# Optimization experiments

Hardware: AMD Instinct MI355X
Metric: run time of the kernel (lower is better)

Reference implementation:

```python
import jax, jax.numpy as jnp
import numpy as np

N = 100000   # nodes
E = 1600000  # edges
R = 500      # relation types
D = 128      # in_ent_feats == out_ent_feats
H = 8        # heads
Dh = 16      # head dim
DFF = 4 * D  # feed-forward hidden
HOPS = 5
ALPHA = 0.15
SLOPE = 0.2
EPS = 1e-5


def setup_inputs() -> dict:
    key = jax.random.key(0)
    ks = jax.random.split(key, 12)
    s = 0.05  # small-init scale
    return {
        "ent_feat": jax.random.normal(ks[0], (N, D), jnp.float32),
        "rel_feat": jax.random.normal(ks[1], (R, D), jnp.float32),
        "src": jax.random.randint(ks[2], (E,), 0, N),
        "dst": jax.random.randint(ks[3], (E,), 0, N),
        "e_type": jax.random.randint(ks[4], (E,), 0, R),
        "ln1_g": jnp.ones((D,), jnp.float32),
        "ln1_b": jnp.zeros((D,), jnp.float32),
        "W_ent": jax.random.normal(ks[5], (D, H * Dh), jnp.float32) * s,
        "W_rel": jax.random.normal(ks[6], (D, H * Dh), jnp.float32) * s,
        "attn_h": jax.random.normal(ks[7], (1, H, Dh), jnp.float32) * s,
        "attn_t": jax.random.normal(ks[8], (1, H, Dh), jnp.float32) * s,
        "attn_r": jax.random.normal(ks[9], (1, H, Dh), jnp.float32) * s,
        "ln2_g": jnp.ones((H * Dh,), jnp.float32),
        "ln2_b": jnp.zeros((H * Dh,), jnp.float32),
        "W1": jax.random.normal(ks[10], (H * Dh, DFF), jnp.float32) * s,
        "b1": jnp.zeros((DFF,), jnp.float32),
        "W2": jax.random.normal(ks[11], (DFF, H * Dh), jnp.float32) * s,
        "b2": jnp.zeros((H * Dh,), jnp.float32),
    }


def _ln(x, g, b):
    mu = x.mean(-1, keepdims=True)
    var = x.var(-1, keepdims=True)
    return (x - mu) * jax.lax.rsqrt(var + EPS) * g + b


def reference(ent_feat, rel_feat, src, dst, e_type,
              ln1_g, ln1_b, W_ent, W_rel, attn_h, attn_t, attn_r,
              ln2_g, ln2_b, W1, b1, W2, b2):
    # graph layer norm (dropout is identity at eval)
    h = _ln(ent_feat, ln1_g, ln1_b)                       # [N, D]
    feat = (h @ W_ent).reshape(N, H, Dh)                  # [N, H, Dh]
    frel = (rel_feat @ W_rel).reshape(R, H, Dh)           # [R, H, Dh]
    eh = (feat * attn_h).sum(-1)                          # [N, H]
    et = (feat * attn_t).sum(-1)                          # [N, H]
    er = (frel * attn_r).sum(-1)[e_type]                  # [E, H]
    # edge scores: u_add_v + relation term, leaky relu
    e = eh[src] + et[dst] + er                            # [E, H]
    e = jnp.where(e > 0, e, SLOPE * e)
    # edge softmax over incoming edges of each dst node
    m = jax.ops.segment_max(e, dst, num_segments=N)       # [N, H]
    ex = jnp.exp(e - m[dst])
    ssum = jax.ops.segment_sum(ex, dst, num_segments=N)
    a = ex / ssum[dst]                                    # [E, H]
    # PPR diffusion
    feat0 = feat
    f = feat0
    for _ in range(HOPS):
        msg = f[src] * a[:, :, None]                      # [E, H, Dh]
        agg = jax.ops.segment_sum(msg, dst, num_segments=N)
        f = (1.0 - ALPHA) * agg + ALPHA * feat0
    # residual (Identity since in == out)
    rst = f + h.reshape(N, H, Dh)
    rst = rst.reshape(N, H * Dh)
    # feed-forward sublayer with residual
    y = _ln(rst, ln2_g, ln2_b)
    ff = jax.nn.relu(y @ W1 + b1) @ W2 + b2
    return ff + rst
```

## Files before the change

kernel.cpp:

```cpp
#include <hip/hip_runtime.h>
#include <hip/hip_bf16.h>
#include <math.h>

#define N_NODES 100000
#define N_EDGES 1600000
#define N_REL   500
#define DIM     128
#define NHEAD   8
#define DFF     512
#define ALPHA   0.15f
#define SLOPE   0.2f
#define LN_EPS  1e-5f

#define SCHUNK   1024
#define NSCANBLK ((N_NODES + SCHUNK - 1) / SCHUNK)

typedef unsigned short u16;
typedef unsigned int   u32;

typedef __attribute__((ext_vector_type(8))) short  bf16x8;
typedef __attribute__((ext_vector_type(4))) float  f32x4;

__device__ __forceinline__ float bf2f(u16 u) {
    return __uint_as_float(((u32)u) << 16);
}
__device__ __forceinline__ u16 f2bf(float f) {
    __hip_bfloat16 b = __float2bfloat16(f);
    return *reinterpret_cast<u16*>(&b);
}
__device__ __forceinline__ u32 pack2(float a, float b) {
    return (u32)f2bf(a) | ((u32)f2bf(b) << 16);
}

__global__ void zero_k(int* __restrict__ p, int n) {
    int i = blockIdx.x * blockDim.x + threadIdx.x;
    if (i < n) p[i] = 0;
}

__global__ void swz1_k(const float* __restrict__ W1, u16* __restrict__ W1s) {
    const int i = blockIdx.x * 256 + threadIdx.x;
    const int k = i >> 9, n = i & 511;
    W1s[n * DIM + k] = f2bf(W1[i]);
}
__global__ void swz2_k(const float* __restrict__ W2, u16* __restrict__ W2s) {
    const int i = blockIdx.x * 256 + threadIdx.x;
    const int k = i >> 7, n = i & 127;
    W2s[n * DFF + k] = f2bf(W2[i]);
}
__global__ void swze_k(const float* __restrict__ W, u16* __restrict__ Ws) {
    const int i = blockIdx.x * 256 + threadIdx.x;
    const int k = i >> 7, n = i & 127;
    Ws[n * DIM + k] = f2bf(W[i]);
}

__global__ __launch_bounds__(128) void ln1_k(const float* __restrict__ x,
        const float* __restrict__ g, const float* __restrict__ b,
        float* __restrict__ h) {
    const int n = blockIdx.x, t = threadIdx.x;
    const float v = x[n * DIM + t];
    float s = v, q = v * v;
#pragma unroll
    for (int off = 32; off > 0; off >>= 1) {
        s += __shfl_xor(s, off, 64);
        q += __shfl_xor(q, off, 64);
    }
    __shared__ float ss[2], qq[2];
    if ((t & 63) == 0) { ss[t >> 6] = s; qq[t >> 6] = q; }
    __syncthreads();
    s = ss[0] + ss[1]; q = qq[0] + qq[1];
    const float mu  = s * (1.0f / 128.0f);
    const float var = q * (1.0f / 128.0f) - mu * mu;
    const float rs  = rsqrtf(fmaxf(var, 0.f) + LN_EPS);
    h[n * DIM + t] = (v - mu) * rs * g[t] + b[t];
}

#define HP 136
__global__ __launch_bounds__(256) void proj_k(const float* __restrict__ h,
        const u16* __restrict__ Wes,
        u16* __restrict__ feat0) {
    __shared__ u16 hsb[32 * HP];
    const int t   = threadIdx.x;
    const int n0b = blockIdx.x * 32;

    {
        const int sr = t >> 3;
        const int sc = (t & 7) * 16;
        const float* hrow = &h[(size_t)(n0b + sr) * DIM + sc];
        u16* drow = &hsb[sr * HP + sc];
#pragma unroll
        for (int i = 0; i < 4; ++i) {
            const float4 hv = ((const float4*)hrow)[i];
            ushort4 o;
            o.x = f2bf(hv.x); o.y = f2bf(hv.y); o.z = f2bf(hv.z); o.w = f2bf(hv.w);
            ((ushort4*)drow)[i] = o;
        }
    }
    __syncthreads();

    const int wv   = t >> 6;
    const int lane = t & 63;
    const int lm   = lane & 15;
    const int q4   = lane >> 4;
    const int mrow = (wv & 1) * 16;
    const int chalf = (wv >> 1) * 64;

    bf16x8 afr[4];
#pragma unroll
    for (int kt = 0; kt < 4; ++kt)
        afr[kt] = *(const bf16x8*)&hsb[(mrow + lm) * HP + kt * 32 + q4 * 8];

#pragma unroll
    for (int nt = 0; nt < 4; ++nt) {
        const int c0 = chalf + nt * 16;
        f32x4 acc = {0.f, 0.f, 0.f, 0.f};
#pragma unroll
        for (int kt = 0; kt < 4; ++kt) {
            const bf16x8 bfr = *(const bf16x8*)&Wes[(c0 + lm) * DIM + kt * 32 + q4 * 8];
            acc = __builtin_amdgcn_mfma_f32_16x16x32_bf16(afr[kt], bfr, acc, 0, 0, 0);
        }
#pragma unroll
        for (int r = 0; r < 4; ++r)
            feat0[(size_t)(n0b + mrow + q4 * 4 + r) * DIM + c0 + lm] = f2bf(acc[r]);
    }
}

__global__ __launch_bounds__(256) void eh_k(const u16* __restrict__ feat0,
        const float* __restrict__ attn_h, const float* __restrict__ attn_t,
        float* __restrict__ eh, float* __restrict__ et) {
    __shared__ float ahs[DIM], ats[DIM];
    const int t = threadIdx.x;
    if (t < DIM) { ahs[t] = attn_h[t]; ats[t] = attn_t[t]; }
    __syncthreads();
    const int idx  = blockIdx.x * 256 + t;
    const int n    = idx >> 3;
    const int head = idx & 7;
    const u16* fp = &feat0[(size_t)n * DIM + head * 16];
    float sh = 0.f, st = 0.f;
#pragma unroll
    for (int i = 0; i < 4; ++i) {
        const ushort4 f4 = ((const ushort4*)fp)[i];
        const int c = head * 16 + i * 4;
        sh += bf2f(f4.x) * ahs[c+0] + bf2f(f4.y) * ahs[c+1]
            + bf2f(f4.z) * ahs[c+2] + bf2f(f4.w) * ahs[c+3];
        st += bf2f(f4.x) * ats[c+0] + bf2f(f4.y) * ats[c+1]
            + bf2f(f4.z) * ats[c+2] + bf2f(f4.w) * ats[c+3];
    }
    eh[idx] = sh;
    et[idx] = st;
}

__global__ __launch_bounds__(128) void rel_k(const float* __restrict__ rel_feat,
        const float* __restrict__ W,
        const float* __restrict__ attn_r, float* __restrict__ er) {
    __shared__ float rf[DIM];
    __shared__ float pr[DIM];
    const int r = blockIdx.x, t = threadIdx.x;
    rf[t] = rel_feat[r * DIM + t];
    __syncthreads();
    float acc = 0.f;
    for (int d = 0; d < DIM; ++d) acc += rf[d] * W[d * DIM + t];
    pr[t] = acc * attn_r[t];
    __syncthreads();
    if (t < NHEAD) {
        float s = 0.f;
        for (int i = 0; i < 16; ++i) s += pr[t * 16 + i];
        er[r * NHEAD + t] = s;
    }
}

__global__ void count_k(const int* __restrict__ dst, int* __restrict__ counts) {
    int e = blockIdx.x * blockDim.x + threadIdx.x;
    if (e < N_EDGES) atomicAdd(&counts[dst[e]], 1);
}

__global__ __launch_bounds__(256) void scan1_k(const int* __restrict__ counts,
        int* __restrict__ offsets, int* __restrict__ blk_sums, int n) {
    __shared__ int wsum[4];
    const int t = threadIdx.x, lane = t & 63, wid = t >> 6;
    const int base = blockIdx.x * SCHUNK + t * 4;
    int v0 = 0, v1 = 0, v2 = 0, v3 = 0;
    if (base + 3 < n) {
        const int4 c4 = *(const int4*)&counts[base];
        v0 = c4.x; v1 = c4.y; v2 = c4.z; v3 = c4.w;
    } else {
        if (base + 0 < n) v0 = counts[base + 0];
        if (base + 1 < n) v1 = counts[base + 1];
        if (base + 2 < n) v2 = counts[base + 2];
        if (base + 3 < n) v3 = counts[base + 3];
    }
    const int s4 = v0 + v1 + v2 + v3;
    int incl = s4;
#pragma unroll
    for (int off = 1; off < 64; off <<= 1) {
        const int tt = __shfl_up(incl, off, 64);
        if (lane >= off) incl += tt;
    }
    if (lane == 63) wsum[wid] = incl;
    __syncthreads();
    int wbase = 0;
#pragma unroll
    for (int w = 0; w < 4; ++w) if (w < wid) wbase += wsum[w];
    const int excl = wbase + incl - s4;
    if (base + 0 < n) offsets[base + 0] = excl;
    if (base + 1 < n) offsets[base + 1] = excl + v0;
    if (base + 2 < n) offsets[base + 2] = excl + v0 + v1;
    if (base + 3 < n) offsets[base + 3] = excl + v0 + v1 + v2;
    if (t == 255) blk_sums[blockIdx.x] = wbase + incl;
}

__global__ __launch_bounds__(128) void scan2_k(const int* __restrict__ blk_sums,
        int* __restrict__ blk_off, int* __restrict__ offsets, int nblk, int n) {
    const int t = threadIdx.x;
    const int v = (t < nblk) ? blk_sums[t] : 0;
    int incl = v;
#pragma unroll
    for (int off = 1; off < 64; off <<= 1) {
        const int tt = __shfl_up(incl, off, 64);
        if ((t & 63) >= off) incl += tt;
    }
    __shared__ int w0sum;
    if (t == 63) w0sum = incl;
    __syncthreads();
    int x = incl - v;
    if (t >= 64) x += w0sum;
    if (t < nblk) blk_off[t] = x;
    if (t == nblk - 1) offsets[n] = x + v;
}

__global__ __launch_bounds__(256) void scan3_k(int* __restrict__ offsets,
        int* __restrict__ cursor, const int* __restrict__ blk_off, int n) {
    const int add  = blk_off[blockIdx.x];
    const int base = blockIdx.x * SCHUNK + threadIdx.x * 4;
#pragma unroll
    for (int j = 0; j < 4; ++j) {
        const int i = base + j;
        if (i < n) {
            const int o = offsets[i] + add;
            offsets[i] = o;
            cursor[i]  = o;
        }
    }
}

__global__ void scatter_k(const int* __restrict__ src, const int* __restrict__ dst,
        const int* __restrict__ etype,
        int* __restrict__ cursor, u32* __restrict__ csr_se) {
    const int e = blockIdx.x * blockDim.x + threadIdx.x;
    if (e >= N_EDGES) return;
    const int s = src[e], d = dst[e], r = etype[e];
    const int pos = atomicAdd(&cursor[d], 1);
    if (pos < 0 || pos >= N_EDGES) return;
    csr_se[pos] = (u32)s | ((u32)r << 17);
}

__global__ __launch_bounds__(256) void softmax_k(const int* __restrict__ offsets,
        const u32* __restrict__ csr_se,
        const float* __restrict__ eh, const float* __restrict__ et,
        const float* __restrict__ er,
        u16* __restrict__ csr_ab, float* __restrict__ inv_buf) {
    const int n = blockIdx.x * 4 + (threadIdx.x >> 6);
    const int beg = offsets[n], end = offsets[n + 1];
    const int lane = threadIdx.x & 63;
    const int k  = lane & 7;
    const int eo = lane >> 3;
    const float etk = et[n * NHEAD + k];
    float m = -1e30f;
    for (int e = beg + eo; e < end; e += 8) {
        const u32 se = csr_se[e];
        const int s = se & 0x1FFFF;
        const int r = se >> 17;
        float sc = eh[s * NHEAD + k] + etk + er[r * NHEAD + k];
        sc = sc > 0.f ? sc : SLOPE * sc;
        m = fmaxf(m, sc);
    }
    m = fmaxf(m, __shfl_xor(m, 8, 64));
    m = fmaxf(m, __shfl_xor(m, 16, 64));
    m = fmaxf(m, __shfl_xor(m, 32, 64));
    float ssum = 0.f;
    for (int e = beg + eo; e < end; e += 8) {
        const u32 se = csr_se[e];
        const int s = se & 0x1FFFF;
        const int r = se >> 17;
        float sc = eh[s * NHEAD + k] + etk + er[r * NHEAD + k];
        sc = sc > 0.f ? sc : SLOPE * sc;
        const float ex = expf(sc - m);
        csr_ab[(size_t)e * NHEAD + k] = f2bf(ex);
        ssum += ex;
    }
    ssum += __shfl_xor(ssum, 8, 64);
    ssum += __shfl_xor(ssum, 16, 64);
    ssum += __shfl_xor(ssum, 32, 64);
    const float inv = 1.f / fmaxf(ssum, 1e-20f);
    if (lane < 8) inv_buf[n * NHEAD + lane] = inv;
}

__global__ __launch_bounds__(256) void hop_k(const u16* __restrict__ f_in,
        u16* __restrict__ f_out, const u16* __restrict__ feat0,
        const int* __restrict__ offsets, const u32* __restrict__ csr_se,
        const u16* __restrict__ csr_ab, const float* __restrict__ inv_buf) {
    const int n    = blockIdx.x * 4 + (threadIdx.x >> 6);
    const int lane = threadIdx.x & 63;
    const int li   = lane & 15;
    const int grp  = lane >> 4;
    const int hsel = li >> 1;
    const int beg = offsets[n], end = offsets[n + 1];
    const int deg = end - beg;

    float acc[8];
#pragma unroll
    for (int j = 0; j < 8; ++j) acc[j] = 0.f;

    const int nfull = deg >> 4;
    int e0 = beg;
    for (int i = 0; i < nfull; ++i, e0 += 16) {
        const u32 se16 = csr_se[e0 + li];
#pragma unroll
        for (int u = 0; u < 4; ++u) {
            const int eu = e0 + u * 4 + grp;
            const u32 se = __shfl(se16, u * 4 + grp, 16);
            const int s  = (int)(se & 0x1FFFF);
            const float a = bf2f(csr_ab[(size_t)eu * NHEAD + hsel]);
            const bf16x8 row = *(const bf16x8*)&f_in[(size_t)s * DIM + li * 8];
#pragma unroll
            for (int j = 0; j < 8; ++j)
                acc[j] += a * bf2f((u16)row[j]);
        }
    }
    for (int e = e0 + grp; e < end; e += 4) {
        const u32 se = csr_se[e];
        const int s  = (int)(se & 0x1FFFF);
        const float a = bf2f(csr_ab[(size_t)e * NHEAD + hsel]);
        const bf16x8 row = *(const bf16x8*)&f_in[(size_t)s * DIM + li * 8];
#pragma unroll
        for (int j = 0; j < 8; ++j)
            acc[j] += a * bf2f((u16)row[j]);
    }
#pragma unroll
    for (int j = 0; j < 8; ++j) {
        acc[j] += __shfl_xor(acc[j], 16, 64);
        acc[j] += __shfl_xor(acc[j], 32, 64);
    }
    if (lane < 16) {
        const float iv = inv_buf[n * NHEAD + hsel];
        const bf16x8 p = *(const bf16x8*)&feat0[(size_t)n * DIM + li * 8];
        bf16x8 o;
#pragma unroll
        for (int j = 0; j < 8; ++j)
            o[j] = (short)f2bf((1.f - ALPHA) * acc[j] * iv + ALPHA * bf2f((u16)p[j]));
        *(bf16x8*)&f_out[(size_t)n * DIM + li * 8] = o;
    }
}

#define YP 136
#define ZP 520
__global__ __launch_bounds__(256) void ffn_k(const u16* __restrict__ f,
        const float* __restrict__ h,
        const float* __restrict__ g2, const float* __restrict__ b2ln,
        const u16* __restrict__ W1s,
        const float* __restrict__ b1,
        const u16* __restrict__ W2s,
        const float* __restrict__ b2,
        float* __restrict__ out) {
    __shared__ u16 ysb[32 * YP];
    __shared__ u16 zsb[32 * ZP];
    __shared__ float red[32][8];
    __shared__ float red2[32][8];
    __shared__ float mu_s[32], rs_s[32];

    const int t   = threadIdx.x;
    const int n0b = blockIdx.x * 32;

    const int an = t >> 3;
    const int ap = t & 7;
    float rv[16];
    {
        const int gbase = (n0b + an) * DIM + ap * 16;
#pragma unroll
        for (int i = 0; i < 4; ++i) {
            const ushort4 fu = *(const ushort4*)&f[gbase + i * 4];
            const float4  hv = *(const float4*)&h[gbase + i * 4];
            rv[i * 4 + 0] = bf2f(fu.x) + hv.x;
            rv[i * 4 + 1] = bf2f(fu.y) + hv.y;
            rv[i * 4 + 2] = bf2f(fu.z) + hv.z;
            rv[i * 4 + 3] = bf2f(fu.w) + hv.w;
        }
        float s = 0.f, q = 0.f;
#pragma unroll
        for (int i = 0; i < 16; ++i) { s += rv[i]; q += rv[i] * rv[i]; }
        red[an][ap] = s; red2[an][ap] = q;
    }
    __syncthreads();
    if (t < 32) {
        float s = 0.f, q = 0.f;
#pragma unroll
        for (int i = 0; i < 8; ++i) { s += red[t][i]; q += red2[t][i]; }
        const float mu  = s * (1.0f / 128.0f);
        const float var = q * (1.0f / 128.0f) - mu * mu;
        mu_s[t] = mu;
        rs_s[t] = rsqrtf(fmaxf(var, 0.f) + LN_EPS);
    }
    __syncthreads();
    {
        const float mu = mu_s[an], rs = rs_s[an];
#pragma unroll
        for (int i = 0; i < 4; ++i) {
            ushort4 yo;
            const int c = ap * 16 + i * 4;
            yo.x = f2bf((rv[i*4+0] - mu) * rs * g2[c+0] + b2ln[c+0]);
            yo.y = f2bf((rv[i*4+1] - mu) * rs * g2[c+1] + b2ln[c+1]);
            yo.z = f2bf((rv[i*4+2] - mu) * rs * g2[c+2] + b2ln[c+2]);
            yo.w = f2bf((rv[i*4+3] - mu) * rs * g2[c+3] + b2ln[c+3]);
            *(ushort4*)&ysb[an * YP + c] = yo;
        }
    }
    __syncthreads();

    const int wv   = t >> 6;
    const int lane = t & 63;
    const int lm   = lane & 15;
    const int q4   = lane >> 4;

    bf16x8 afr[2][4];
#pragma unroll
    for (int mt = 0; mt < 2; ++mt)
#pragma unroll
        for (int kt = 0; kt < 4; ++kt)
            afr[mt][kt] = *(const bf16x8*)&ysb[(mt * 16 + lm) * YP + kt * 32 + q4 * 8];

    for (int nt = 0; nt < 8; ++nt) {
        const int n0 = wv * 128 + nt * 16;
        f32x4 acc0 = {0.f, 0.f, 0.f, 0.f};
        f32x4 acc1 = {0.f, 0.f, 0.f, 0.f};
#pragma unroll
        for (int kt = 0; kt < 4; ++kt) {
            const bf16x8 bfr = *(const bf16x8*)&W1s[(n0 + lm) * DIM + kt * 32 + q4 * 8];
            acc0 = __builtin_amdgcn_mfma_f32_16x16x32_bf16(afr[0][kt], bfr, acc0, 0, 0, 0);
            acc1 = __builtin_amdgcn_mfma_f32_16x16x32_bf16(afr[1][kt], bfr, acc1, 0, 0, 0);
        }
        const float bias = b1[n0 + lm];
#pragma unroll
        for (int r = 0; r < 4; ++r) {
            zsb[(q4 * 4 + r) * ZP + n0 + lm]        = f2bf(fmaxf(acc0[r] + bias, 0.f));
            zsb[(16 + q4 * 4 + r) * ZP + n0 + lm]   = f2bf(fmaxf(acc1[r] + bias, 0.f));
        }
    }
    __syncthreads();

    f32x4 acc[2][2];
#pragma unroll
    for (int i = 0; i < 2; ++i)
#pragma unroll
        for (int j = 0; j < 2; ++j)
            acc[i][j] = (f32x4){0.f, 0.f, 0.f, 0.f};
    const int c0 = wv * 32;
    for (int kt = 0; kt < 16; ++kt) {
        const bf16x8 a0 = *(const bf16x8*)&zsb[(lm) * ZP + kt * 32 + q4 * 8];
        const bf16x8 a1 = *(const bf16x8*)&zsb[(16 + lm) * ZP + kt * 32 + q4 * 8];
        const bf16x8 b0 = *(const bf16x8*)&W2s[(c0 + lm) * DFF + kt * 32 + q4 * 8];
        const bf16x8 b1f = *(const bf16x8*)&W2s[(c0 + 16 + lm) * DFF + kt * 32 + q4 * 8];
        acc[0][0] = __builtin_amdgcn_mfma_f32_16x16x32_bf16(a0, b0, acc[0][0], 0, 0, 0);
        acc[0][1] = __builtin_amdgcn_mfma_f32_16x16x32_bf16(a0, b1f, acc[0][1], 0, 0, 0);
        acc[1][0] = __builtin_amdgcn_mfma_f32_16x16x32_bf16(a1, b0, acc[1][0], 0, 0, 0);
        acc[1][1] = __builtin_amdgcn_mfma_f32_16x16x32_bf16(a1, b1f, acc[1][1], 0, 0, 0);
    }

#pragma unroll
    for (int ntile = 0; ntile < 2; ++ntile) {
        const int col = c0 + ntile * 16 + lm;
        const float bias = b2[col];
#pragma unroll
        for (int mt = 0; mt < 2; ++mt) {
#pragma unroll
            for (int r = 0; r < 4; ++r) {
                const int row  = mt * 16 + q4 * 4 + r;
                const int gidx = (n0b + row) * DIM + col;
                out[gidx] = acc[mt][ntile][r] + bias + bf2f(f[gidx]) + h[gidx];
            }
        }
    }
}

extern "C" void kernel_launch(void* const* d_in, const int* in_sizes, int n_in,
                              void* d_out, int out_size, void* d_ws, size_t ws_size,
                              hipStream_t stream) {
    const float* ent_feat = (const float*)d_in[0];
    const float* rel_feat = (const float*)d_in[1];
    const int*   src      = (const int*)d_in[2];
    const int*   dst      = (const int*)d_in[3];
    const int*   e_type   = (const int*)d_in[4];
    const float* ln1_g    = (const float*)d_in[5];
    const float* ln1_b    = (const float*)d_in[6];
    const float* W_ent    = (const float*)d_in[7];
    const float* W_rel    = (const float*)d_in[8];
    const float* attn_h   = (const float*)d_in[9];
    const float* attn_t   = (const float*)d_in[10];
    const float* attn_r   = (const float*)d_in[11];
    const float* ln2_g    = (const float*)d_in[12];
    const float* ln2_b    = (const float*)d_in[13];
    const float* W1       = (const float*)d_in[14];
    const float* b1       = (const float*)d_in[15];
    const float* W2       = (const float*)d_in[16];
    const float* b2       = (const float*)d_in[17];
    float* out = (float*)d_out;

    char* ws = (char*)d_ws;
    size_t used = 0;
    auto alloc = [&](size_t bytes) -> char* {
        char* p = ws + used;
        used += (bytes + 255) & ~(size_t)255;
        return p;
    };
    float* h       = (float*)alloc((size_t)N_NODES * DIM * 4);
    u16*   feat0   = (u16*)  alloc((size_t)N_NODES * DIM * 2);
    u16*   fA      = (u16*)  alloc((size_t)N_NODES * DIM * 2);
    u16*   fB      = (u16*)  alloc((size_t)N_NODES * DIM * 2);
    u16*   csr_ab  = (u16*)  alloc((size_t)N_EDGES * NHEAD * 2);
    float* eh      = (float*)alloc((size_t)N_NODES * NHEAD * 4);
    float* et      = (float*)alloc((size_t)N_NODES * NHEAD * 4);
    float* inv_buf = (float*)alloc((size_t)N_NODES * NHEAD * 4);
    u32*   csr_se  = (u32*)  alloc((size_t)N_EDGES * 4);
    int*   counts  = (int*)  alloc((size_t)N_NODES * 4);
    int*   offsets = (int*)  alloc((size_t)(N_NODES + 1) * 4);
    int*   cursor  = (int*)  alloc((size_t)N_NODES * 4);
    float* er      = (float*)alloc((size_t)N_REL * NHEAD * 4);
    u16*   W1s     = (u16*)  alloc((size_t)DIM * DFF * 2);
    u16*   W2s     = (u16*)  alloc((size_t)DFF * DIM * 2);
    u16*   Wes     = (u16*)  alloc((size_t)DIM * DIM * 2);
    int*   blk_sums= (int*)  alloc((size_t)NSCANBLK * 4);
    int*   blk_off = (int*)  alloc((size_t)NSCANBLK * 4);

    if (used > ws_size) return;

    swz1_k<<<DIM * DFF / 256, 256, 0, stream>>>(W1, W1s);
    swz2_k<<<DFF * DIM / 256, 256, 0, stream>>>(W2, W2s);
    swze_k<<<DIM * DIM / 256, 256, 0, stream>>>(W_ent, Wes);

    ln1_k<<<N_NODES, 128, 0, stream>>>(ent_feat, ln1_g, ln1_b, h);
    proj_k<<<N_NODES / 32, 256, 0, stream>>>(h, Wes, feat0);
    eh_k<<<N_NODES * NHEAD / 256, 256, 0, stream>>>(feat0, attn_h, attn_t, eh, et);
    rel_k<<<N_REL, 128, 0, stream>>>(rel_feat, W_rel, attn_r, er);

    zero_k<<<(N_NODES + 255) / 256, 256, 0, stream>>>(counts, N_NODES);
    count_k<<<(N_EDGES + 255) / 256, 256, 0, stream>>>(dst, counts);
    scan1_k<<<NSCANBLK, 256, 0, stream>>>(counts, offsets, blk_sums, N_NODES);
    scan2_k<<<1, 128, 0, stream>>>(blk_sums, blk_off, offsets, NSCANBLK, N_NODES);
    scan3_k<<<NSCANBLK, 256, 0, stream>>>(offsets, cursor, blk_off, N_NODES);
    scatter_k<<<(N_EDGES + 255) / 256, 256, 0, stream>>>(src, dst, e_type,
                                                         cursor, csr_se);
    softmax_k<<<N_NODES / 4, 256, 0, stream>>>(offsets, csr_se, eh, et, er,
                                               csr_ab, inv_buf);

    hop_k<<<N_NODES / 4, 256, 0, stream>>>(feat0, fA, feat0, offsets, csr_se, csr_ab, inv_buf);
    hop_k<<<N_NODES / 4, 256, 0, stream>>>(fA, fB, feat0, offsets, csr_se, csr_ab, inv_buf);
    hop_k<<<N_NODES / 4, 256, 0, stream>>>(fB, fA, feat0, offsets, csr_se, csr_ab, inv_buf);
    hop_k<<<N_NODES / 4, 256, 0, stream>>>(fA, fB, feat0, offsets, csr_se, csr_ab, inv_buf);
    hop_k<<<N_NODES / 4, 256, 0, stream>>>(fB, fA, feat0, offsets, csr_se, csr_ab, inv_buf);

    ffn_k<<<N_NODES / 32, 256, 0, stream>>>(fA, h, ln2_g, ln2_b, W1s, b1, W2s, b2,
                                            out);
}
```

Baseline: 932.6 us.

## Window CSR scatter by destination range and batch gathers in hop kernel

The CSR scatter now runs as a 2D grid: each block scans one edge chunk and handles only edges whose destination falls in one of 8 node windows. Atomics and csr writes then land in a narrower address range per block, which should improve locality. The cost is that every block re-reads dst for its whole chunk, so dst is read 8 times. Separately, the hop kernel processes 32 edges per iteration, issuing 8 row gathers before accumulating to raise memory-level parallelism, at the cost of more registers.

```diff
diff --git a/kernel.cpp b/kernel.cpp
--- a/kernel.cpp
+++ b/kernel.cpp
@@ -15,6 +15,11 @@
 #define SCHUNK   1024
 #define NSCANBLK ((N_NODES + SCHUNK - 1) / SCHUNK)
 
+#define NWIN    8
+#define WNODES  12500
+#define NECHUNK 256
+#define ECHUNK  (N_EDGES / NECHUNK)
+
 typedef unsigned short u16;
 typedef unsigned int   u32;
 
@@ -27,9 +32,6 @@
 __device__ __forceinline__ u16 f2bf(float f) {
     __hip_bfloat16 b = __float2bfloat16(f);
     return *reinterpret_cast<u16*>(&b);
-}
-__device__ __forceinline__ u32 pack2(float a, float b) {
-    return (u32)f2bf(a) | ((u32)f2bf(b) << 16);
 }
 
 __global__ void zero_k(int* __restrict__ p, int n) {
@@ -242,15 +244,25 @@
     }
 }
 
-__global__ void scatter_k(const int* __restrict__ src, const int* __restrict__ dst,
-        const int* __restrict__ etype,
+__global__ __launch_bounds__(256) void scatter_k(const int* __restrict__ src,
+        const int* __restrict__ dst, const int* __restrict__ etype,
         int* __restrict__ cursor, u32* __restrict__ csr_se) {
-    const int e = blockIdx.x * blockDim.x + threadIdx.x;
-    if (e >= N_EDGES) return;
-    const int s = src[e], d = dst[e], r = etype[e];
-    const int pos = atomicAdd(&cursor[d], 1);
-    if (pos < 0 || pos >= N_EDGES) return;
-    csr_se[pos] = (u32)s | ((u32)r << 17);
+    const int b  = blockIdx.x;
+    const int w  = b & (NWIN - 1);
+    const int r  = b >> 3;
+    const int lo = w * WNODES, hi = lo + WNODES;
+    const int base = r * ECHUNK;
+    for (int i = threadIdx.x; i < ECHUNK; i += 256) {
+        const int e = base + i;
+        const int d = dst[e];
+        if (d >= lo && d < hi) {
+            const int s   = src[e];
+            const int rel = etype[e];
+            const int pos = atomicAdd(&cursor[d], 1);
+            if (pos >= 0 && pos < N_EDGES)
+                csr_se[pos] = (u32)s | ((u32)rel << 17);
+        }
+    }
 }
 
 __global__ __launch_bounds__(256) void softmax_k(const int* __restrict__ offsets,
@@ -304,36 +316,56 @@
     const int grp  = lane >> 4;
     const int hsel = li >> 1;
     const int beg = offsets[n], end = offsets[n + 1];
-    const int deg = end - beg;
 
     float acc[8];
 #pragma unroll
     for (int j = 0; j < 8; ++j) acc[j] = 0.f;
 
-    const int nfull = deg >> 4;
     int e0 = beg;
-    for (int i = 0; i < nfull; ++i, e0 += 16) {
+    for (; e0 + 32 <= end; e0 += 32) {
+        const u32 seA = csr_se[e0 + li];
+        const u32 seB = csr_se[e0 + 16 + li];
+        bf16x8 row[8];
+        float  a[8];
+#pragma unroll
+        for (int u = 0; u < 4; ++u) {
+            const int s = (int)(__shfl(seA, u * 4 + grp, 16) & 0x1FFFF);
+            row[u] = *(const bf16x8*)&f_in[(size_t)s * DIM + li * 8];
+            a[u]   = bf2f(csr_ab[(size_t)(e0 + u * 4 + grp) * NHEAD + hsel]);
+        }
+#pragma unroll
+        for (int u = 0; u < 4; ++u) {
+            const int s = (int)(__shfl(seB, u * 4 + grp, 16) & 0x1FFFF);
+            row[4 + u] = *(const bf16x8*)&f_in[(size_t)s * DIM + li * 8];
+            a[4 + u]   = bf2f(csr_ab[(size_t)(e0 + 16 + u * 4 + grp) * NHEAD + hsel]);
+        }
+#pragma unroll
+        for (int u = 0; u < 8; ++u)
+#pragma unroll
+            for (int j = 0; j < 8; ++j)
+                acc[j] += a[u] * bf2f((u16)row[u][j]);
+    }
+    for (; e0 + 16 <= end; e0 += 16) {
         const u32 se16 = csr_se[e0 + li];
 #pragma unroll
         for (int u = 0; u < 4; ++u) {
             const int eu = e0 + u * 4 + grp;
-            const u32 se = __shfl(se16, u * 4 + grp, 16);
-            const int s  = (int)(se & 0x1FFFF);
-            const float a = bf2f(csr_ab[(size_t)eu * NHEAD + hsel]);
-            const bf16x8 row = *(const bf16x8*)&f_in[(size_t)s * DIM + li * 8];
+            const int s  = (int)(__shfl(se16, u * 4 + grp, 16) & 0x1FFFF);
+            const float av = bf2f(csr_ab[(size_t)eu * NHEAD + hsel]);
+            const bf16x8 rw = *(const bf16x8*)&f_in[(size_t)s * DIM + li * 8];
 #pragma unroll
             for (int j = 0; j < 8; ++j)
-                acc[j] += a * bf2f((u16)row[j]);
+                acc[j] += av * bf2f((u16)rw[j]);
         }
     }
     for (int e = e0 + grp; e < end; e += 4) {
         const u32 se = csr_se[e];
         const int s  = (int)(se & 0x1FFFF);
-        const float a = bf2f(csr_ab[(size_t)e * NHEAD + hsel]);
-        const bf16x8 row = *(const bf16x8*)&f_in[(size_t)s * DIM + li * 8];
+        const float av = bf2f(csr_ab[(size_t)e * NHEAD + hsel]);
+        const bf16x8 rw = *(const bf16x8*)&f_in[(size_t)s * DIM + li * 8];
 #pragma unroll
         for (int j = 0; j < 8; ++j)
-            acc[j] += a * bf2f((u16)row[j]);
+            acc[j] += av * bf2f((u16)rw[j]);
     }
 #pragma unroll
     for (int j = 0; j < 8; ++j) {
@@ -545,8 +577,8 @@
     scan1_k<<<NSCANBLK, 256, 0, stream>>>(counts, offsets, blk_sums, N_NODES);
     scan2_k<<<1, 128, 0, stream>>>(blk_sums, blk_off, offsets, NSCANBLK, N_NODES);
     scan3_k<<<NSCANBLK, 256, 0, stream>>>(offsets, cursor, blk_off, N_NODES);
-    scatter_k<<<(N_EDGES + 255) / 256, 256, 0, stream>>>(src, dst, e_type,
-                                                         cursor, csr_se);
+    scatter_k<<<NECHUNK * NWIN, 256, 0, stream>>>(src, dst, e_type,
+                                                  cursor, csr_se);
     softmax_k<<<N_NODES / 4, 256, 0, stream>>>(offsets, csr_se, eh, et, er,
                                                csr_ab, inv_buf);
 
```

New measurement: 936.1 us. No clear change (+0.4%).

## Window CSR scatter by destination range and shrink FFN tile to 16 nodes

Applied to the files above, without the earlier changes.

The edge scatter now has each block scan one edge chunk and keep only edges whose destination falls in one of 8 node windows. This localizes the atomic cursor traffic and the CSR writes, at the cost of reading dst 8 times. The FFN kernel now processes 16 nodes per block instead of 32, which doubles the block count and cuts shared memory use. It also replaces the LDS reduction and two barriers for layer norm with wave shuffles. The smaller tile gives less weight reuse per block.

```diff
diff --git a/kernel.cpp b/kernel.cpp
--- a/kernel.cpp
+++ b/kernel.cpp
@@ -15,6 +15,13 @@
 #define SCHUNK   1024
 #define NSCANBLK ((N_NODES + SCHUNK - 1) / SCHUNK)
 
+#define NWIN    8
+#define WNODES  12500
+#define NECHUNK 256
+#define ECHUNK  (N_EDGES / NECHUNK)
+
+#define FNODES  16
+
 typedef unsigned short u16;
 typedef unsigned int   u32;
 
@@ -27,9 +34,6 @@
 __device__ __forceinline__ u16 f2bf(float f) {
     __hip_bfloat16 b = __float2bfloat16(f);
     return *reinterpret_cast<u16*>(&b);
-}
-__device__ __forceinline__ u32 pack2(float a, float b) {
-    return (u32)f2bf(a) | ((u32)f2bf(b) << 16);
 }
 
 __global__ void zero_k(int* __restrict__ p, int n) {
@@ -242,15 +246,25 @@
     }
 }
 
-__global__ void scatter_k(const int* __restrict__ src, const int* __restrict__ dst,
-        const int* __restrict__ etype,
+__global__ __launch_bounds__(256) void scatter_k(const int* __restrict__ src,
+        const int* __restrict__ dst, const int* __restrict__ etype,
         int* __restrict__ cursor, u32* __restrict__ csr_se) {
-    const int e = blockIdx.x * blockDim.x + threadIdx.x;
-    if (e >= N_EDGES) return;
-    const int s = src[e], d = dst[e], r = etype[e];
-    const int pos = atomicAdd(&cursor[d], 1);
-    if (pos < 0 || pos >= N_EDGES) return;
-    csr_se[pos] = (u32)s | ((u32)r << 17);
+    const int b  = blockIdx.x;
+    const int w  = b & (NWIN - 1);
+    const int r  = b >> 3;
+    const int lo = w * WNODES, hi = lo + WNODES;
+    const int base = r * ECHUNK;
+    for (int i = threadIdx.x; i < ECHUNK; i += 256) {
+        const int e = base + i;
+        const int d = dst[e];
+        if (d >= lo && d < hi) {
+            const int s   = src[e];
+            const int rel = etype[e];
+            const int pos = atomicAdd(&cursor[d], 1);
+            if (pos >= 0 && pos < N_EDGES)
+                csr_se[pos] = (u32)s | ((u32)rel << 17);
+        }
+    }
 }
 
 __global__ __launch_bounds__(256) void softmax_k(const int* __restrict__ offsets,
@@ -361,107 +375,89 @@
         const u16* __restrict__ W2s,
         const float* __restrict__ b2,
         float* __restrict__ out) {
-    __shared__ u16 ysb[32 * YP];
-    __shared__ u16 zsb[32 * ZP];
-    __shared__ float red[32][8];
-    __shared__ float red2[32][8];
-    __shared__ float mu_s[32], rs_s[32];
-
-    const int t   = threadIdx.x;
-    const int n0b = blockIdx.x * 32;
-
-    const int an = t >> 3;
-    const int ap = t & 7;
-    float rv[16];
+    __shared__ u16 ysb[FNODES * YP];
+    __shared__ u16 zsb[FNODES * ZP];
+
+    const int t    = threadIdx.x;
+    const int n0b  = blockIdx.x * FNODES;
+    const int wv   = t >> 6;
+    const int lane = t & 63;
+
     {
-        const int gbase = (n0b + an) * DIM + ap * 16;
-#pragma unroll
-        for (int i = 0; i < 4; ++i) {
-            const ushort4 fu = *(const ushort4*)&f[gbase + i * 4];
-            const float4  hv = *(const float4*)&h[gbase + i * 4];
-            rv[i * 4 + 0] = bf2f(fu.x) + hv.x;
-            rv[i * 4 + 1] = bf2f(fu.y) + hv.y;
-            rv[i * 4 + 2] = bf2f(fu.z) + hv.z;
-            rv[i * 4 + 3] = bf2f(fu.w) + hv.w;
-        }
+        const int node = t >> 4;
+        const int cp   = (t & 15) * 8;
+        const int gbase = (n0b + node) * DIM + cp;
+        const ushort4 fu0 = *(const ushort4*)&f[gbase];
+        const ushort4 fu1 = *(const ushort4*)&f[gbase + 4];
+        const float4  hv0 = *(const float4*)&h[gbase];
+        const float4  hv1 = *(const float4*)&h[gbase + 4];
+        float rv[8];
+        rv[0] = bf2f(fu0.x) + hv0.x; rv[1] = bf2f(fu0.y) + hv0.y;
+        rv[2] = bf2f(fu0.z) + hv0.z; rv[3] = bf2f(fu0.w) + hv0.w;
+        rv[4] = bf2f(fu1.x) + hv1.x; rv[5] = bf2f(fu1.y) + hv1.y;
+        rv[6] = bf2f(fu1.z) + hv1.z; rv[7] = bf2f(fu1.w) + hv1.w;
         float s = 0.f, q = 0.f;
 #pragma unroll
-        for (int i = 0; i < 16; ++i) { s += rv[i]; q += rv[i] * rv[i]; }
-        red[an][ap] = s; red2[an][ap] = q;
-    }
-    __syncthreads();
-    if (t < 32) {
-        float s = 0.f, q = 0.f;
-#pragma unroll
-        for (int i = 0; i < 8; ++i) { s += red[t][i]; q += red2[t][i]; }
+        for (int i = 0; i < 8; ++i) { s += rv[i]; q += rv[i] * rv[i]; }
+        s += __shfl_xor(s, 1, 64); q += __shfl_xor(q, 1, 64);
+        s += __shfl_xor(s, 2, 64); q += __shfl_xor(q, 2, 64);
+        s += __shfl_xor(s, 4, 64); q += __shfl_xor(q, 4, 64);
+        s += __shfl_xor(s, 8, 64); q += __shfl_xor(q, 8, 64);
         const float mu  = s * (1.0f / 128.0f);
         const float var = q * (1.0f / 128.0f) - mu * mu;
-        mu_s[t] = mu;
-        rs_s[t] = rsqrtf(fmaxf(var, 0.f) + LN_EPS);
-    }
-    __syncthreads();
+        const float rs  = rsqrtf(fmaxf(var, 0.f) + LN_EPS);
+        ushort4 yo0, yo1;
+        yo0.x = f2bf((rv[0] - mu) * rs * g2[cp+0] + b2ln[cp+0]);
+        yo0.y = f2bf((rv[1] - mu) * rs * g2[cp+1] + b2ln[cp+1]);
+        yo0.z = f2bf((rv[2] - mu) * rs * g2[cp+2] + b2ln[cp+2]);
+        yo0.w = f2bf((rv[3] - mu) * rs * g2[cp+3] + b2ln[cp+3]);
+        yo1.x = f2bf((rv[4] - mu) * rs * g2[cp+4] + b2ln[cp+4]);
+        yo1.y = f2bf((rv[5] - mu) * rs * g2[cp+5] + b2ln[cp+5]);
+        yo1.z = f2bf((rv[6] - mu) * rs * g2[cp+6] + b2ln[cp+6]);
+        yo1.w = f2bf((rv[7] - mu) * rs * g2[cp+7] + b2ln[cp+7]);
+        *(ushort4*)&ysb[node * YP + cp]     = yo0;
+        *(ushort4*)&ysb[node * YP + cp + 4] = yo1;
+    }
+    __syncthreads();
+
+    const int lm = lane & 15;
+    const int q4 = lane >> 4;
+
     {
-        const float mu = mu_s[an], rs = rs_s[an];
-#pragma unroll
-        for (int i = 0; i < 4; ++i) {
-            ushort4 yo;
-            const int c = ap * 16 + i * 4;
-            yo.x = f2bf((rv[i*4+0] - mu) * rs * g2[c+0] + b2ln[c+0]);
-            yo.y = f2bf((rv[i*4+1] - mu) * rs * g2[c+1] + b2ln[c+1]);
-            yo.z = f2bf((rv[i*4+2] - mu) * rs * g2[c+2] + b2ln[c+2]);
-            yo.w = f2bf((rv[i*4+3] - mu) * rs * g2[c+3] + b2ln[c+3]);
-            *(ushort4*)&ysb[an * YP + c] = yo;
-        }
-    }
-    __syncthreads();
-
-    const int wv   = t >> 6;
-    const int lane = t & 63;
-    const int lm   = lane & 15;
-    const int q4   = lane >> 4;
-
-    bf16x8 afr[2][4];
-#pragma unroll
-    for (int mt = 0; mt < 2; ++mt)
+        bf16x8 afr[4];
 #pragma unroll
         for (int kt = 0; kt < 4; ++kt)
-            afr[mt][kt] = *(const bf16x8*)&ysb[(mt * 16 + lm) * YP + kt * 32 + q4 * 8];
-
-    for (int nt = 0; nt < 8; ++nt) {
-        const int n0 = wv * 128 + nt * 16;
-        f32x4 acc0 = {0.f, 0.f, 0.f, 0.f};
-        f32x4 acc1 = {0.f, 0.f, 0.f, 0.f};
-#pragma unroll
-        for (int kt = 0; kt < 4; ++kt) {
-            const bf16x8 bfr = *(const bf16x8*)&W1s[(n0 + lm) * DIM + kt * 32 + q4 * 8];
-            acc0 = __builtin_amdgcn_mfma_f32_16x16x32_bf16(afr[0][kt], bfr, acc0, 0, 0, 0);
-            acc1 = __builtin_amdgcn_mfma_f32_16x16x32_bf16(afr[1][kt], bfr, acc1, 0, 0, 0);
-        }
-        const float bias = b1[n0 + lm];
-#pragma unroll
-        for (int r = 0; r < 4; ++r) {
-            zsb[(q4 * 4 + r) * ZP + n0 + lm]        = f2bf(fmaxf(acc0[r] + bias, 0.f));
-            zsb[(16 + q4 * 4 + r) * ZP + n0 + lm]   = f2bf(fmaxf(acc1[r] + bias, 0.f));
-        }
-    }
-    __syncthreads();
-
-    f32x4 acc[2][2];
-#pragma unroll
-    for (int i = 0; i < 2; ++i)
-#pragma unroll
-        for (int j = 0; j < 2; ++j)
-            acc[i][j] = (f32x4){0.f, 0.f, 0.f, 0.f};
+            afr[kt] = *(const bf16x8*)&ysb[lm * YP + kt * 32 + q4 * 8];
+
+        const int cw = wv * 128;
+#pragma unroll
+        for (int nt = 0; nt < 8; ++nt) {
+            const int n0 = cw + nt * 16;
+            f32x4 acc0 = {0.f, 0.f, 0.f, 0.f};
+#pragma unroll
+            for (int kt = 0; kt < 4; ++kt) {
+                const bf16x8 bfr = *(const bf16x8*)&W1s[(n0 + lm) * DIM + kt * 32 + q4 * 8];
+                acc0 = __builtin_amdgcn_mfma_f32_16x16x32_bf16(afr[kt], bfr, acc0, 0, 0, 0);
+            }
+            const float bias = b1[n0 + lm];
+#pragma unroll
+            for (int r = 0; r < 4; ++r)
+                zsb[(q4 * 4 + r) * ZP + n0 + lm] = f2bf(fmaxf(acc0[r] + bias, 0.f));
+        }
+    }
+    __syncthreads();
+
+    f32x4 acc[2];
+    acc[0] = (f32x4){0.f, 0.f, 0.f, 0.f};
+    acc[1] = (f32x4){0.f, 0.f, 0.f, 0.f};
     const int c0 = wv * 32;
+#pragma unroll
     for (int kt = 0; kt < 16; ++kt) {
-        const bf16x8 a0 = *(const bf16x8*)&zsb[(lm) * ZP + kt * 32 + q4 * 8];
-        const bf16x8 a1 = *(const bf16x8*)&zsb[(16 + lm) * ZP + kt * 32 + q4 * 8];
-        const bf16x8 b0 = *(const bf16x8*)&W2s[(c0 + lm) * DFF + kt * 32 + q4 * 8];
+        const bf16x8 a0  = *(const bf16x8*)&zsb[lm * ZP + kt * 32 + q4 * 8];
+        const bf16x8 b0  = *(const bf16x8*)&W2s[(c0 + lm) * DFF + kt * 32 + q4 * 8];
         const bf16x8 b1f = *(const bf16x8*)&W2s[(c0 + 16 + lm) * DFF + kt * 32 + q4 * 8];
-        acc[0][0] = __builtin_amdgcn_mfma_f32_16x16x32_bf16(a0, b0, acc[0][0], 0, 0, 0);
-        acc[0][1] = __builtin_amdgcn_mfma_f32_16x16x32_bf16(a0, b1f, acc[0][1], 0, 0, 0);
-        acc[1][0] = __builtin_amdgcn_mfma_f32_16x16x32_bf16(a1, b0, acc[1][0], 0, 0, 0);
-        acc[1][1] = __builtin_amdgcn_mfma_f32_16x16x32_bf16(a1, b1f, acc[1][1], 0, 0, 0);
+        acc[0] = __builtin_amdgcn_mfma_f32_16x16x32_bf16(a0, b0,  acc[0], 0, 0, 0);
+        acc[1] = __builtin_amdgcn_mfma_f32_16x16x32_bf16(a0, b1f, acc[1], 0, 0, 0);
     }
 
 #pragma unroll
@@ -469,13 +465,10 @@
         const int col = c0 + ntile * 16 + lm;
         const float bias = b2[col];
 #pragma unroll
-        for (int mt = 0; mt < 2; ++mt) {
-#pragma unroll
-            for (int r = 0; r < 4; ++r) {
-                const int row  = mt * 16 + q4 * 4 + r;
-                const int gidx = (n0b + row) * DIM + col;
-                out[gidx] = acc[mt][ntile][r] + bias + bf2f(f[gidx]) + h[gidx];
-            }
+        for (int r = 0; r < 4; ++r) {
+            const int row  = q4 * 4 + r;
+            const int gidx = (n0b + row) * DIM + col;
+            out[gidx] = acc[ntile][r] + bias + bf2f(f[gidx]) + h[gidx];
         }
     }
 }
@@ -545,8 +538,8 @@
     scan1_k<<<NSCANBLK, 256, 0, stream>>>(counts, offsets, blk_sums, N_NODES);
     scan2_k<<<1, 128, 0, stream>>>(blk_sums, blk_off, offsets, NSCANBLK, N_NODES);
     scan3_k<<<NSCANBLK, 256, 0, stream>>>(offsets, cursor, blk_off, N_NODES);
-    scatter_k<<<(N_EDGES + 255) / 256, 256, 0, stream>>>(src, dst, e_type,
-                                                         cursor, csr_se);
+    scatter_k<<<NECHUNK * NWIN, 256, 0, stream>>>(src, dst, e_type,
+                                                  cursor, csr_se);
     softmax_k<<<N_NODES / 4, 256, 0, stream>>>(offsets, csr_se, eh, et, er,
                                                csr_ab, inv_buf);
 
@@ -556,6 +549,6 @@
     hop_k<<<N_NODES / 4, 256, 0, stream>>>(fA, fB, feat0, offsets, csr_se, csr_ab, inv_buf);
     hop_k<<<N_NODES / 4, 256, 0, stream>>>(fB, fA, feat0, offsets, csr_se, csr_ab, inv_buf);
 
-    ffn_k<<<N_NODES / 32, 256, 0, stream>>>(fA, h, ln2_g, ln2_b, W1s, b1, W2s, b2,
-                                            out);
-}
+    ffn_k<<<N_NODES / FNODES, 256, 0, stream>>>(fA, h, ln2_g, ln2_b, W1s, b1, W2s, b2,
+                                                out);
+}
```

After: 969.8 us. +4.0%, slower.
